# Optimization experiments

Hardware: AMD Instinct MI355X
Metric: run time of the kernel (lower is better)

Reference implementation:

```python
import jax, jax.numpy as jnp
import numpy as np

NUM_VARS = 256
BATCH = 131072


def setup_inputs() -> dict:
    key = jax.random.key(0)
    k1, k2 = jax.random.split(key)
    z_exogenous = jax.random.normal(k1, (BATCH, NUM_VARS), dtype=jnp.float32)
    # Learnable adjacency parameter; small init like the torch prior (~0.01 scale).
    A_raw = jax.random.normal(k2, (NUM_VARS, NUM_VARS), dtype=jnp.float32) * 0.01
    return {"z_exogenous": z_exogenous, "A_raw": A_raw}


def reference(z_exogenous, A_raw):
    # A = tril(A_raw, -1): strictly lower triangular (no threshold in forward).
    n = A_raw.shape[0]
    A = jnp.tril(A_raw, -1)
    # M = I - A^T is upper triangular with unit diagonal and is shared across
    # the whole batch, so solve the triangular system once for all RHS columns
    # instead of a batched LU (same math as torch.linalg.solve).
    M = jnp.eye(n, dtype=A_raw.dtype) - A.T          # [n, n] upper triangular
    z_causal = jax.scipy.linalg.solve_triangular(M, z_exogenous.T, lower=False).T  # [B, n]
    return z_causal
```

## Files before the change

### kernel.cpp

```cpp
#include <hip/hip_runtime.h>
#include <hip/hip_bf16.h>


typedef __bf16 bf16x8 __attribute__((ext_vector_type(8)));
typedef float f32x4 __attribute__((ext_vector_type(4)));

__device__ __forceinline__ unsigned short f2bf(float f) {
    union { float f; unsigned u; } v; v.f = f;
    unsigned u = v.u;
    u += 0x7FFFu + ((u >> 16) & 1u);
    return (unsigned short)(u >> 16);
}
__device__ __forceinline__ bf16x8 pack8(float4 a, float4 b) {
    union { bf16x8 v; __hip_bfloat162 h[4]; } u;
    u.h[0] = __float22bfloat162_rn(make_float2(a.x, a.y));
    u.h[1] = __float22bfloat162_rn(make_float2(a.z, a.w));
    u.h[2] = __float22bfloat162_rn(make_float2(b.x, b.y));
    u.h[3] = __float22bfloat162_rn(make_float2(b.z, b.w));
    return u.v;
}

#define AST 258
__global__ __launch_bounds__(256) void make_G3(const float* __restrict__ A,
                                               unsigned short* __restrict__ Gt) {
    __shared__ unsigned short As[256 * AST];
    const int tid = threadIdx.x;
    const int l = tid & 63;
    const int wv = tid >> 6;

    for (int it = 0; it < 64; ++it) {
        const int r = it * 4 + wv;
        const int c0 = l * 4;
        float4 v = *(const float4*)(A + r * 256 + c0);
        *(ushort2*)(&As[r * AST + c0])     = make_ushort2(f2bf(v.x), f2bf(v.y));
        *(ushort2*)(&As[r * AST + c0 + 2]) = make_ushort2(f2bf(v.z), f2bf(v.w));
    }
    __syncthreads();
    if (wv != 0) return;

    const int c = blockIdx.x;
    float p[4];
#pragma unroll
    for (int k = 0; k < 4; ++k) p[k] = (64 * k + l == c) ? 1.f : 0.f;

#pragma unroll
    for (int kb = 0; kb < 4; ++kb) {
#pragma unroll 8
        for (int i2 = 0; i2 < 32; ++i2) {
            unsigned u[4];
#pragma unroll
            for (int k = 0; k < 4; ++k)
                if (k >= kb)
                    u[k] = *(const unsigned*)(&As[(64 * k + l) * AST + kb * 64 + 2 * i2]);
            const int t0 = 2 * i2, t1 = t0 + 1;
            float s0 = __int_as_float(__builtin_amdgcn_readlane(__float_as_int(p[kb]), t0));
            p[kb] += (l > t0 ? __int_as_float(u[kb] << 16) : 0.f) * s0;
#pragma unroll
            for (int k = 0; k < 4; ++k)
                if (k > kb) p[k] += __int_as_float(u[k] << 16) * s0;
            float s1 = __int_as_float(__builtin_amdgcn_readlane(__float_as_int(p[kb]), t1));
            p[kb] += (l > t1 ? __int_as_float(u[kb] & 0xffff0000u) : 0.f) * s1;
#pragma unroll
            for (int k = 0; k < 4; ++k)
                if (k > kb) p[k] += __int_as_float(u[k] & 0xffff0000u) * s1;
        }
    }
#pragma unroll
    for (int k = 0; k < 4; ++k)
        Gt[c * 256 + 64 * k + l] = f2bf(p[k]);
}

__global__ __launch_bounds__(512, 2) void scm_gemm3(const float* __restrict__ Z,
                                                    const unsigned short* __restrict__ Gt,
                                                    float* __restrict__ Out) {
    __shared__ __align__(16) unsigned short Gs[256 * 264];
    const int tid = threadIdx.x;
    const int lane = tid & 63;
    const int wave = tid >> 6;
    const int n = lane & 15;
    const int quad = lane >> 4;
    const size_t m0 = (size_t)blockIdx.x * 256 + wave * 32;

    float4 zf[2][16];
    const float* zb0 = Z + (m0 + n) * 256 + quad * 8;
    const float* zb1 = zb0 + 16 * 256;
#pragma unroll
    for (int kk = 0; kk < 8; ++kk) {
        zf[0][2 * kk]     = *(const float4*)(zb0 + kk * 32);
        zf[0][2 * kk + 1] = *(const float4*)(zb0 + kk * 32 + 4);
    }
#pragma unroll
    for (int kk = 0; kk < 8; ++kk) {
        zf[1][2 * kk]     = *(const float4*)(zb1 + kk * 32);
        zf[1][2 * kk + 1] = *(const float4*)(zb1 + kk * 32 + 4);
    }

#pragma unroll
    for (int it = 0; it < 16; ++it) {
        const int chunk = it * 512 + tid;
        const int row = chunk >> 5;
        const int g = chunk & 31;
        const int gs = g ^ ((row & 3) << 2);
        uint4 v = *(const uint4*)(Gt + row * 256 + g * 8);
        *(uint4*)(&Gs[(row * 33 + gs) * 8]) = v;
    }
    __syncthreads();

    bf16x8 af[2][8];
#pragma unroll
    for (int h = 0; h < 2; ++h)
#pragma unroll
        for (int kk = 0; kk < 8; ++kk)
            af[h][kk] = pack8(zf[h][2 * kk], zf[h][2 * kk + 1]);

    f32x4 acc[2][16];
#pragma unroll
    for (int h = 0; h < 2; ++h)
#pragma unroll
        for (int nt = 0; nt < 16; ++nt) {
            f32x4 zero = {0.f, 0.f, 0.f, 0.f};
            acc[h][nt] = zero;
        }
    const int swz = (n & 3) << 2;
#pragma unroll
    for (int kk = 0; kk < 8; ++kk) {
#pragma unroll
        for (int nt = 0; nt < 16; ++nt) {
            const bf16x8 bfr = *(const bf16x8*)(
                &Gs[((nt * 16 + n) * 33 + ((kk * 4 + quad) ^ swz)) * 8]);
            acc[0][nt] = __builtin_amdgcn_mfma_f32_16x16x32_bf16(
                af[0][kk], bfr, acc[0][nt], 0, 0, 0);
            acc[1][nt] = __builtin_amdgcn_mfma_f32_16x16x32_bf16(
                af[1][kk], bfr, acc[1][nt], 0, 0, 0);
        }
    }

#pragma unroll
    for (int h = 0; h < 2; ++h)
#pragma unroll
        for (int nt = 0; nt < 16; ++nt)
#pragma unroll
            for (int r = 0; r < 4; ++r)
                Out[(m0 + h * 16 + quad * 4 + r) * 256 + nt * 16 + n] = acc[h][nt][r];
}

extern "C" void kernel_launch(void* const* d_in, const int* in_sizes, int n_in,
                              void* d_out, int out_size, void* d_ws, size_t ws_size,
                              hipStream_t stream) {
    const float* Z = (const float*)d_in[0];
    const float* A = (const float*)d_in[1];
    float* Out = (float*)d_out;
    unsigned short* Gt = (unsigned short*)d_ws;

    hipLaunchKernelGGL(make_G3, dim3(256), dim3(256), 0, stream, A, Gt);
    hipLaunchKernelGGL(scm_gemm3, dim3(512), dim3(512), 0, stream, Z, Gt, Out);
}
```

Baseline: 267.6 us.

## Split GEMM output columns across blocks and software-pipeline Z loads over row tiles

The GEMM kernel now has each block handle half of the output columns (128) for 512 rows, processed as four 128-row tiles per wave-group. Only half of G goes to LDS, which halves shared memory and allows four blocks per CU instead of two. Z loads for the next K-half or tile are issued before the current MFMAs so memory latency overlaps with compute. Each Z row is now read twice, once by each of the two column-half blocks, which adds global traffic in exchange for the smaller LDS footprint and fewer accumulator registers.

```diff
diff --git a/kernel.cpp b/kernel.cpp
--- a/kernel.cpp
+++ b/kernel.cpp
@@ -70,78 +70,92 @@
         Gt[c * 256 + 64 * k + l] = f2bf(p[k]);
 }
 
-__global__ __launch_bounds__(512, 2) void scm_gemm3(const float* __restrict__ Z,
+__global__ __launch_bounds__(512, 4) void scm_gemm4(const float* __restrict__ Z,
                                                     const unsigned short* __restrict__ Gt,
                                                     float* __restrict__ Out) {
-    __shared__ __align__(16) unsigned short Gs[256 * 264];
+    __shared__ __align__(16) unsigned short Gs[128 * 256];
     const int tid = threadIdx.x;
     const int lane = tid & 63;
     const int wave = tid >> 6;
     const int n = lane & 15;
     const int quad = lane >> 4;
-    const size_t m0 = (size_t)blockIdx.x * 256 + wave * 32;
-
-    float4 zf[2][16];
-    const float* zb0 = Z + (m0 + n) * 256 + quad * 8;
-    const float* zb1 = zb0 + 16 * 256;
-#pragma unroll
-    for (int kk = 0; kk < 8; ++kk) {
-        zf[0][2 * kk]     = *(const float4*)(zb0 + kk * 32);
-        zf[0][2 * kk + 1] = *(const float4*)(zb0 + kk * 32 + 4);
-    }
-#pragma unroll
-    for (int kk = 0; kk < 8; ++kk) {
-        zf[1][2 * kk]     = *(const float4*)(zb1 + kk * 32);
-        zf[1][2 * kk + 1] = *(const float4*)(zb1 + kk * 32 + 4);
-    }
+    const int bn = (blockIdx.x & 1) * 128;
+    const size_t blockRow = (size_t)(blockIdx.x >> 1) * 512;
 
 #pragma unroll
-    for (int it = 0; it < 16; ++it) {
+    for (int it = 0; it < 8; ++it) {
         const int chunk = it * 512 + tid;
         const int row = chunk >> 5;
         const int g = chunk & 31;
-        const int gs = g ^ ((row & 3) << 2);
-        uint4 v = *(const uint4*)(Gt + row * 256 + g * 8);
-        *(uint4*)(&Gs[(row * 33 + gs) * 8]) = v;
+        const int gs = g ^ (row & 7);
+        uint4 v = *(const uint4*)(Gt + (bn + row) * 256 + g * 8);
+        *(uint4*)(&Gs[row * 256 + gs * 8]) = v;
     }
     __syncthreads();
 
-    bf16x8 af[2][8];
+    const int swz = n & 7;
+    const float* zbase = Z + (blockRow + wave * 16 + n) * 256 + quad * 8;
+    float* obase = Out + (blockRow + wave * 16 + quad * 4) * 256 + bn + n;
+
+    f32x4 acc[8];
 #pragma unroll
-    for (int h = 0; h < 2; ++h)
-#pragma unroll
-        for (int kk = 0; kk < 8; ++kk)
-            af[h][kk] = pack8(zf[h][2 * kk], zf[h][2 * kk + 1]);
-
-    f32x4 acc[2][16];
-#pragma unroll
-    for (int h = 0; h < 2; ++h)
-#pragma unroll
-        for (int nt = 0; nt < 16; ++nt) {
-            f32x4 zero = {0.f, 0.f, 0.f, 0.f};
-            acc[h][nt] = zero;
-        }
-    const int swz = (n & 3) << 2;
-#pragma unroll
-    for (int kk = 0; kk < 8; ++kk) {
-#pragma unroll
-        for (int nt = 0; nt < 16; ++nt) {
-            const bf16x8 bfr = *(const bf16x8*)(
-                &Gs[((nt * 16 + n) * 33 + ((kk * 4 + quad) ^ swz)) * 8]);
-            acc[0][nt] = __builtin_amdgcn_mfma_f32_16x16x32_bf16(
-                af[0][kk], bfr, acc[0][nt], 0, 0, 0);
-            acc[1][nt] = __builtin_amdgcn_mfma_f32_16x16x32_bf16(
-                af[1][kk], bfr, acc[1][nt], 0, 0, 0);
-        }
+    for (int nt = 0; nt < 8; ++nt) {
+        f32x4 zero = {0.f, 0.f, 0.f, 0.f};
+        acc[nt] = zero;
     }
 
+    float4 zf[8];
 #pragma unroll
-    for (int h = 0; h < 2; ++h)
+    for (int kk = 0; kk < 4; ++kk) {
+        zf[2 * kk]     = *(const float4*)(zbase + kk * 32);
+        zf[2 * kk + 1] = *(const float4*)(zbase + kk * 32 + 4);
+    }
+
+    for (int i = 0; i < 4; ++i) {
+        const float* zi = zbase + (size_t)i * 128 * 256;
+        bf16x8 af[4];
 #pragma unroll
-        for (int nt = 0; nt < 16; ++nt)
+        for (int kk = 0; kk < 4; ++kk) af[kk] = pack8(zf[2 * kk], zf[2 * kk + 1]);
 #pragma unroll
-            for (int r = 0; r < 4; ++r)
-                Out[(m0 + h * 16 + quad * 4 + r) * 256 + nt * 16 + n] = acc[h][nt][r];
+        for (int kk = 0; kk < 4; ++kk) {
+            zf[2 * kk]     = *(const float4*)(zi + 128 + kk * 32);
+            zf[2 * kk + 1] = *(const float4*)(zi + 128 + kk * 32 + 4);
+        }
+#pragma unroll
+        for (int kk = 0; kk < 4; ++kk)
+#pragma unroll
+            for (int nt = 0; nt < 8; ++nt) {
+                const bf16x8 b = *(const bf16x8*)(
+                    &Gs[(nt * 16 + n) * 256 + ((kk * 4 + quad) ^ swz) * 8]);
+                acc[nt] = __builtin_amdgcn_mfma_f32_16x16x32_bf16(af[kk], b, acc[nt], 0, 0, 0);
+            }
+#pragma unroll
+        for (int kk = 0; kk < 4; ++kk) af[kk] = pack8(zf[2 * kk], zf[2 * kk + 1]);
+        if (i < 3) {
+            const float* zn = zbase + (size_t)(i + 1) * 128 * 256;
+#pragma unroll
+            for (int kk = 0; kk < 4; ++kk) {
+                zf[2 * kk]     = *(const float4*)(zn + kk * 32);
+                zf[2 * kk + 1] = *(const float4*)(zn + kk * 32 + 4);
+            }
+        }
+#pragma unroll
+        for (int kk = 0; kk < 4; ++kk)
+#pragma unroll
+            for (int nt = 0; nt < 8; ++nt) {
+                const bf16x8 b = *(const bf16x8*)(
+                    &Gs[(nt * 16 + n) * 256 + (((16 + kk * 4 + quad)) ^ swz) * 8]);
+                acc[nt] = __builtin_amdgcn_mfma_f32_16x16x32_bf16(af[kk], b, acc[nt], 0, 0, 0);
+            }
+        float* oi = obase + (size_t)i * 128 * 256;
+#pragma unroll
+        for (int nt = 0; nt < 8; ++nt)
+#pragma unroll
+            for (int r = 0; r < 4; ++r) {
+                oi[(size_t)r * 256 + nt * 16] = acc[nt][r];
+                acc[nt][r] = 0.f;
+            }
+    }
 }
 
 extern "C" void kernel_launch(void* const* d_in, const int* in_sizes, int n_in,
@@ -153,5 +167,5 @@
     unsigned short* Gt = (unsigned short*)d_ws;
 
     hipLaunchKernelGGL(make_G3, dim3(256), dim3(256), 0, stream, A, Gt);
-    hipLaunchKernelGGL(scm_gemm3, dim3(512), dim3(512), 0, stream, Z, Gt, Out);
+    hipLaunchKernelGGL(scm_gemm4, dim3(512), dim3(512), 0, stream, Z, Gt, Out);
 }
```

Result: no change. 267.0 us (-0.2%).
